# Optimization experiments

Hardware: AMD Instinct MI355X
Metric: run time of the kernel (lower is better)

The kernel has to match this reference:

```python
import jax, jax.numpy as jnp
import numpy as np

HIDDEN = 2048
EXPERTS = 8
INTER = 1024
TOP_K = 2
AUX_LOSS_WEIGHT = 0.01
TOKENS = 8192


def setup_inputs() -> dict:
    key = jax.random.key(0)
    k_x, k_g, k_w1, k_w2 = jax.random.split(key, 4)
    x = jax.random.normal(k_x, (TOKENS, HIDDEN), dtype=jnp.float32)
    # nn.Linear(hidden, experts, bias=False): weight is [E, H], applied as x @ W^T
    gate_w = jax.random.normal(k_g, (EXPERTS, HIDDEN), dtype=jnp.float32) * 0.02
    w1 = jax.random.normal(k_w1, (EXPERTS, HIDDEN, INTER), dtype=jnp.float32) * 0.02
    w2 = jax.random.normal(k_w2, (EXPERTS, INTER, HIDDEN), dtype=jnp.float32) * 0.02
    return {"x": x, "gate_w": gate_w, "w1": w1, "w2": w2}


def _moe_forward(x, gate_w, w1, w2):
    E = gate_w.shape[0]
    logits = x @ gate_w.T                              # [T, E]
    probs = jax.nn.softmax(logits, axis=-1)            # [T, E]
    topk_w, topk_idx = jax.lax.top_k(probs, TOP_K)     # [T, K]
    topk_w = topk_w / jnp.sum(topk_w, axis=-1, keepdims=True)

    # load-balancing aux loss: E * sum_e f_e * P_e
    one_hot = jax.nn.one_hot(topk_idx, E, dtype=probs.dtype)   # [T, K, E]
    f = jnp.mean(jnp.sum(one_hot, axis=1), axis=0)             # fraction of tokens per expert
    P = jnp.mean(probs, axis=0)                                # mean router prob per expert
    aux_loss = AUX_LOSS_WEIGHT * E * jnp.sum(f * P)

    # grouped expert MLP (dense-over-experts formulation, same math as
    # permute -> grouped GEMM -> unpermute):
    h = jnp.einsum('th,ehi->tei', x, w1)               # [T, E, I]
    h = jax.nn.gelu(h)
    y = jnp.einsum('tei,eih->teh', h, w2)              # [T, E, H]

    # combine: gather each token's top-k expert outputs and weight them
    y_sel = jnp.take_along_axis(y, topk_idx[:, :, None], axis=1)  # [T, K, H]
    out = jnp.sum(y_sel * topk_w[:, :, None], axis=1)             # [T, H]
    return out, aux_loss


def reference(x, gate_w, w1, w2):
    return _moe_forward(x, gate_w, w1, w2)
```

## Files before the change

kernel.cpp:

```cpp
#include <hip/hip_runtime.h>
#include <hip/hip_fp16.h>
#include <cmath>

#define T_TOKENS 8192
#define HID 2048
#define NEXP 8
#define INTERM 1024
#define GATE_NB 2048

typedef _Float16 f16x8 __attribute__((ext_vector_type(8)));
typedef _Float16 f16x4 __attribute__((ext_vector_type(4)));
typedef float f32x4 __attribute__((ext_vector_type(4)));

static __device__ __forceinline__ float gelu_tanh(float v) {
    return 0.5f * v * (1.0f + tanhf(0.79788456080286535588f * (v + 0.044715f * v * v * v)));
}

static __device__ __forceinline__ void glds16(const void* g, void* l) {
    __builtin_amdgcn_global_load_lds((const __attribute__((address_space(1))) void*)g,
                                     (__attribute__((address_space(3))) void*)l, 16, 0, 0);
}

__global__ __launch_bounds__(256) void tconv_kernel(const float* __restrict__ in,
                                                    _Float16* __restrict__ out,
                                                    int R, int C) {
    __shared__ float t[32][33];
    int z = blockIdx.z;
    int r0 = blockIdx.y * 32, c0 = blockIdx.x * 32;
    int tid = threadIdx.x;
    int r = tid >> 3, c4 = (tid & 7) * 4;
    const float4 v = *reinterpret_cast<const float4*>(&in[((size_t)z * R + (r0 + r)) * C + c0 + c4]);
    t[r][c4 + 0] = v.x; t[r][c4 + 1] = v.y; t[r][c4 + 2] = v.z; t[r][c4 + 3] = v.w;
    __syncthreads();
    int oc = tid >> 3;
    int or4 = (tid & 7) * 4;
    f16x4 o;
    o[0] = (_Float16)t[or4 + 0][oc];
    o[1] = (_Float16)t[or4 + 1][oc];
    o[2] = (_Float16)t[or4 + 2][oc];
    o[3] = (_Float16)t[or4 + 3][oc];
    *reinterpret_cast<f16x4*>(&out[((size_t)z * C + (c0 + oc)) * R + r0 + or4]) = o;
}

__global__ __launch_bounds__(256) void gate_kernel(const float* __restrict__ x,
                                                   const float* __restrict__ gw,
                                                   _Float16* __restrict__ xh,
                                                   int* __restrict__ tk_idx, float* __restrict__ tk_w,
                                                   int* __restrict__ part_cnt,
                                                   double* __restrict__ part_sumP)
{
    __shared__ double sds[4][NEXP];
    __shared__ int sci[4][NEXP];
    int w = threadIdx.x >> 6;
    int lane = threadIdx.x & 63;
    int t = blockIdx.x * 4 + w;

    const float4* xr = (const float4*)(x + (size_t)t * HID);
    _Float16* xo = xh + (size_t)t * HID;
    double acc[NEXP];
#pragma unroll
    for (int e = 0; e < NEXP; e++) acc[e] = 0.0;
#pragma unroll
    for (int i = 0; i < HID / 256; i++) {
        float4 xv = xr[i * 64 + lane];
        f16x4 h;
        h[0] = (_Float16)xv.x; h[1] = (_Float16)xv.y;
        h[2] = (_Float16)xv.z; h[3] = (_Float16)xv.w;
        *reinterpret_cast<f16x4*>(xo + i * 256 + lane * 4) = h;
#pragma unroll
        for (int e = 0; e < NEXP; e++) {
            float4 gv = ((const float4*)(gw + (size_t)e * HID))[i * 64 + lane];
            acc[e] += (double)xv.x * (double)gv.x + (double)xv.y * (double)gv.y
                    + (double)xv.z * (double)gv.z + (double)xv.w * (double)gv.w;
        }
    }
#pragma unroll
    for (int e = 0; e < NEXP; e++) {
#pragma unroll
        for (int off = 32; off > 0; off >>= 1) acc[e] += __shfl_xor(acc[e], off, 64);
    }
    double mx = acc[0];
#pragma unroll
    for (int e = 1; e < NEXP; e++) mx = acc[e] > mx ? acc[e] : mx;
    double ex[NEXP];
    double sum = 0.0;
#pragma unroll
    for (int e = 0; e < NEXP; e++) { ex[e] = exp(acc[e] - mx); sum += ex[e]; }
    int i0 = 0;
#pragma unroll
    for (int e = 1; e < NEXP; e++) if (ex[e] > ex[i0]) i0 = e;
    int i1 = (i0 == 0) ? 1 : 0;
#pragma unroll
    for (int e = 0; e < NEXP; e++) if (e != i0 && ex[e] > ex[i1]) i1 = e;
    double p0 = ex[i0], p1 = ex[i1];
    double t2 = p0 + p1;
    if (lane == 0) {
        tk_idx[2 * t] = i0; tk_idx[2 * t + 1] = i1;
        tk_w[2 * t] = (float)(p0 / t2); tk_w[2 * t + 1] = (float)(p1 / t2);
#pragma unroll
        for (int e = 0; e < NEXP; e++) {
            sds[w][e] = ex[e] / sum;
            sci[w][e] = (e == i0 ? 1 : 0) + (e == i1 ? 1 : 0);
        }
    }
    __syncthreads();
    if (threadIdx.x < NEXP) {
        int e = threadIdx.x;
        part_sumP[e * GATE_NB + blockIdx.x] = sds[0][e] + sds[1][e] + sds[2][e] + sds[3][e];
        part_cnt[e * GATE_NB + blockIdx.x]  = sci[0][e] + sci[1][e] + sci[2][e] + sci[3][e];
    }
}

__global__ __launch_bounds__(256) void finalize_kernel(const int* __restrict__ part_cnt,
                                                       const double* __restrict__ part_sumP,
                                                       int* __restrict__ cnt, int* __restrict__ offs,
                                                       int* __restrict__ cursor,
                                                       float* __restrict__ aux_out) {
    __shared__ double swv[4];
    __shared__ int cwv[4];
    __shared__ double sE[NEXP];
    __shared__ int cE[NEXP];
    int w = threadIdx.x >> 6;
    int lane = threadIdx.x & 63;
    for (int e = 0; e < NEXP; e++) {
        double s = 0.0; int c = 0;
        for (int j = threadIdx.x; j < GATE_NB; j += 256) {
            s += part_sumP[e * GATE_NB + j];
            c += part_cnt[e * GATE_NB + j];
        }
#pragma unroll
        for (int off = 32; off > 0; off >>= 1) {
            s += __shfl_xor(s, off, 64);
            c += __shfl_xor(c, off, 64);
        }
        if (lane == 0) { swv[w] = s; cwv[w] = c; }
        __syncthreads();
        if (threadIdx.x == 0) {
            sE[e] = swv[0] + swv[1] + swv[2] + swv[3];
            cE[e] = cwv[0] + cwv[1] + cwv[2] + cwv[3];
        }
        __syncthreads();
    }
    if (threadIdx.x == 0) {
        int off = 0;
        double aux = 0.0;
#pragma unroll
        for (int e = 0; e < NEXP; e++) {
            cnt[e] = cE[e];
            offs[e] = off;
            off += cE[e];
            cursor[e] = 0;
            aux += ((double)cE[e] / (double)T_TOKENS) * (sE[e] / (double)T_TOKENS);
        }
        aux_out[0] = (float)(0.01 * (double)NEXP * aux);
    }
}

__global__ void scatter_kernel(const int* __restrict__ tk_idx, const float* __restrict__ tk_w,
                               const int* __restrict__ offs, int* __restrict__ cursor,
                               int* __restrict__ row_tok, float* __restrict__ row_w,
                               int* __restrict__ tok_row) {
    int t = blockIdx.x * blockDim.x + threadIdx.x;
    int lane = threadIdx.x & 63;
    unsigned long long below = (lane == 0) ? 0ull : ((~0ull) >> (64 - lane));
    for (int k = 0; k < 2; k++) {
        int e = tk_idx[2 * t + k];
        float wv = tk_w[2 * t + k];
        int pos = 0;
#pragma unroll
        for (int ee = 0; ee < NEXP; ee++) {
            unsigned long long m = __ballot(e == ee);
            if (e == ee) {
                int rank = (int)__popcll(m & below);
                int leader = (int)__ffsll((unsigned long long)m) - 1;
                int base = 0;
                if (lane == leader) base = atomicAdd(&cursor[ee], (int)__popcll(m));
                base = __shfl(base, leader, 64);
                pos = base + rank;
            }
        }
        int r = offs[e] + pos;
        row_tok[r] = t;
        row_w[r] = wv;
        tok_row[2 * t + k] = r;
    }
}

__global__ __launch_bounds__(256) void gemm1_kernel(const _Float16* __restrict__ xh,
                                                    const _Float16* __restrict__ w1t,
                                                    const int* __restrict__ cnt, const int* __restrict__ offs,
                                                    const int* __restrict__ row_tok,
                                                    _Float16* __restrict__ hh) {
    int e = blockIdx.z;
    int Ne = cnt[e];
    int m0 = blockIdx.y * 128;
    if (m0 >= Ne) return;
    int base = offs[e];
    int n0 = blockIdx.x * 128;

    __shared__ __align__(16) _Float16 As[128][32];
    __shared__ __align__(16) _Float16 Bs[128][32];

    int tid = threadIdx.x;
    int lane = tid & 63;
    int w = tid >> 6, wm = w >> 1, wn = w & 1;

    int r0 = lane >> 2;
    int kh = (((lane & 3) ^ ((lane >> 3) & 3))) * 8;
    int rowA0 = m0 + w * 32 + r0;      if (rowA0 >= Ne) rowA0 = Ne - 1;
    int rowA1 = m0 + w * 32 + 16 + r0; if (rowA1 >= Ne) rowA1 = Ne - 1;
    int tok0 = row_tok[base + rowA0];
    int tok1 = row_tok[base + rowA1];
    const _Float16* aSrc0 = xh + (size_t)tok0 * HID + kh;
    const _Float16* aSrc1 = xh + (size_t)tok1 * HID + kh;
    const _Float16* bSrc0 = w1t + ((size_t)e * INTERM + n0 + w * 32 + r0) * HID + kh;
    const _Float16* bSrc1 = w1t + ((size_t)e * INTERM + n0 + w * 32 + 16 + r0) * HID + kh;
    _Float16* ldsA0 = &As[w * 32][0];
    _Float16* ldsA1 = &As[w * 32 + 16][0];
    _Float16* ldsB0 = &Bs[w * 32][0];
    _Float16* ldsB1 = &Bs[w * 32 + 16][0];

    f32x4 acc[4][4] = {};
    int fr = lane & 15;
    int fq = lane >> 4;
    int fk = (fq ^ ((fr >> 1) & 3)) * 8;

    for (int k0 = 0; k0 < HID; k0 += 32) {
        glds16(aSrc0 + k0, ldsA0);
        glds16(aSrc1 + k0, ldsA1);
        glds16(bSrc0 + k0, ldsB0);
        glds16(bSrc1 + k0, ldsB1);
        __syncthreads();
        f16x8 a[4], b[4];
#pragma unroll
        for (int mi = 0; mi < 4; mi++) a[mi] = *(const f16x8*)&As[wm * 64 + mi * 16 + fr][fk];
#pragma unroll
        for (int ni = 0; ni < 4; ni++) b[ni] = *(const f16x8*)&Bs[wn * 64 + ni * 16 + fr][fk];
#pragma unroll
        for (int mi = 0; mi < 4; mi++)
#pragma unroll
            for (int ni = 0; ni < 4; ni++)
                acc[mi][ni] = __builtin_amdgcn_mfma_f32_16x16x32_f16(a[mi], b[ni], acc[mi][ni], 0, 0, 0);
        __syncthreads();
    }

    int fq4 = fq * 4;
#pragma unroll
    for (int mi = 0; mi < 4; mi++) {
#pragma unroll
        for (int r = 0; r < 4; r++) {
            int row = m0 + wm * 64 + mi * 16 + fq4 + r;
            if (row < Ne) {
                _Float16* dst = hh + (size_t)(base + row) * INTERM + n0 + wn * 64 + fr;
#pragma unroll
                for (int ni = 0; ni < 4; ni++)
                    dst[ni * 16] = (_Float16)gelu_tanh(acc[mi][ni][r]);
            }
        }
    }
}

__global__ __launch_bounds__(256) void gemm2_kernel(const _Float16* __restrict__ hh,
                                                    const _Float16* __restrict__ w2t,
                                                    const int* __restrict__ cnt, const int* __restrict__ offs,
                                                    _Float16* __restrict__ y) {
    int e = blockIdx.z;
    int Ne = cnt[e];
    int m0 = blockIdx.y * 128;
    if (m0 >= Ne) return;
    int base = offs[e];
    int n0 = blockIdx.x * 128;

    __shared__ __align__(16) _Float16 As[128][32];
    __shared__ __align__(16) _Float16 Bs[128][32];

    int tid = threadIdx.x;
    int lane = tid & 63;
    int w = tid >> 6, wm = w >> 1, wn = w & 1;

    int r0 = lane >> 2;
    int kh = (((lane & 3) ^ ((lane >> 3) & 3))) * 8;
    int rowA0 = m0 + w * 32 + r0;      if (rowA0 >= Ne) rowA0 = Ne - 1;
    int rowA1 = m0 + w * 32 + 16 + r0; if (rowA1 >= Ne) rowA1 = Ne - 1;
    const _Float16* aSrc0 = hh + (size_t)(base + rowA0) * INTERM + kh;
    const _Float16* aSrc1 = hh + (size_t)(base + rowA1) * INTERM + kh;
    const _Float16* bSrc0 = w2t + ((size_t)e * HID + n0 + w * 32 + r0) * INTERM + kh;
    const _Float16* bSrc1 = w2t + ((size_t)e * HID + n0 + w * 32 + 16 + r0) * INTERM + kh;
    _Float16* ldsA0 = &As[w * 32][0];
    _Float16* ldsA1 = &As[w * 32 + 16][0];
    _Float16* ldsB0 = &Bs[w * 32][0];
    _Float16* ldsB1 = &Bs[w * 32 + 16][0];

    f32x4 acc[4][4] = {};
    int fr = lane & 15;
    int fq = lane >> 4;
    int fk = (fq ^ ((fr >> 1) & 3)) * 8;

    for (int k0 = 0; k0 < INTERM; k0 += 32) {
        glds16(aSrc0 + k0, ldsA0);
        glds16(aSrc1 + k0, ldsA1);
        glds16(bSrc0 + k0, ldsB0);
        glds16(bSrc1 + k0, ldsB1);
        __syncthreads();
        f16x8 a[4], b[4];
#pragma unroll
        for (int mi = 0; mi < 4; mi++) a[mi] = *(const f16x8*)&As[wm * 64 + mi * 16 + fr][fk];
#pragma unroll
        for (int ni = 0; ni < 4; ni++) b[ni] = *(const f16x8*)&Bs[wn * 64 + ni * 16 + fr][fk];
#pragma unroll
        for (int mi = 0; mi < 4; mi++)
#pragma unroll
            for (int ni = 0; ni < 4; ni++)
                acc[mi][ni] = __builtin_amdgcn_mfma_f32_16x16x32_f16(a[mi], b[ni], acc[mi][ni], 0, 0, 0);
        __syncthreads();
    }

    int fq4 = fq * 4;
#pragma unroll
    for (int mi = 0; mi < 4; mi++) {
#pragma unroll
        for (int r = 0; r < 4; r++) {
            int row = m0 + wm * 64 + mi * 16 + fq4 + r;
            if (row < Ne) {
                _Float16* dst = y + (size_t)(base + row) * HID + n0 + wn * 64 + fr;
#pragma unroll
                for (int ni = 0; ni < 4; ni++)
                    dst[ni * 16] = (_Float16)acc[mi][ni][r];
            }
        }
    }
}

__global__ __launch_bounds__(256) void combine_kernel(const _Float16* __restrict__ y,
                                                      const int* __restrict__ tok_row,
                                                      const float* __restrict__ tk_w,
                                                      float* __restrict__ out) {
    int t = blockIdx.x;
    int c = threadIdx.x;
    int r0 = tok_row[2 * t], r1 = tok_row[2 * t + 1];
    float w0 = tk_w[2 * t], w1 = tk_w[2 * t + 1];
    f16x8 a = reinterpret_cast<const f16x8*>(y + (size_t)r0 * HID)[c];
    f16x8 b = reinterpret_cast<const f16x8*>(y + (size_t)r1 * HID)[c];
    float4 o0, o1;
    o0.x = w0 * (float)a[0] + w1 * (float)b[0];
    o0.y = w0 * (float)a[1] + w1 * (float)b[1];
    o0.z = w0 * (float)a[2] + w1 * (float)b[2];
    o0.w = w0 * (float)a[3] + w1 * (float)b[3];
    o1.x = w0 * (float)a[4] + w1 * (float)b[4];
    o1.y = w0 * (float)a[5] + w1 * (float)b[5];
    o1.z = w0 * (float)a[6] + w1 * (float)b[6];
    o1.w = w0 * (float)a[7] + w1 * (float)b[7];
    float4* dst = reinterpret_cast<float4*>(out + (size_t)t * HID + c * 8);
    dst[0] = o0;
    dst[1] = o1;
}

extern "C" void kernel_launch(void* const* d_in, const int* in_sizes, int n_in,
                              void* d_out, int out_size, void* d_ws, size_t ws_size,
                              hipStream_t stream) {
    const float* x  = (const float*)d_in[0];
    const float* gw = (const float*)d_in[1];
    const float* w1 = (const float*)d_in[2];
    const float* w2 = (const float*)d_in[3];
    float* out = (float*)d_out;
    char* ws = (char*)d_ws;

    int*    cnt       = (int*)(ws + 0);
    int*    cursor    = (int*)(ws + 64);
    int*    offs      = (int*)(ws + 128);
    int*    part_cnt  = (int*)(ws + 4096);
    double* part_sumP = (double*)(ws + 131072);
    int*    row_tok   = (int*)(ws + 262144);
    float*  row_w     = (float*)(ws + 327680);
    int*    tk_idx    = (int*)(ws + 393216);
    float*  tk_w      = (float*)(ws + 458752);
    int*    tok_row   = (int*)(ws + 524288);
    const size_t OFF = 589824;
    _Float16* xh  = (_Float16*)(ws + OFF);
    _Float16* w1t = (_Float16*)(ws + OFF + (1ull << 25));
    _Float16* w2t = (_Float16*)(ws + OFF + (2ull << 25));
    _Float16* hh  = (_Float16*)(ws + OFF + (3ull << 25));
    _Float16* y   = (_Float16*)(ws + OFF);

    dim3 g1(INTERM / 32, HID / 32, NEXP);
    tconv_kernel<<<g1, 256, 0, stream>>>(w1, w1t, HID, INTERM);
    dim3 g2(HID / 32, INTERM / 32, NEXP);
    tconv_kernel<<<g2, 256, 0, stream>>>(w2, w2t, INTERM, HID);

    gate_kernel<<<GATE_NB, 256, 0, stream>>>(x, gw, xh, tk_idx, tk_w, part_cnt, part_sumP);
    finalize_kernel<<<1, 256, 0, stream>>>(part_cnt, part_sumP, cnt, offs, cursor,
                                           out + (size_t)T_TOKENS * HID);
    scatter_kernel<<<T_TOKENS / 256, 256, 0, stream>>>(tk_idx, tk_w, offs, cursor,
                                                       row_tok, row_w, tok_row);

    dim3 gg1(INTERM / 128, 64, NEXP);
    gemm1_kernel<<<gg1, 256, 0, stream>>>(xh, w1t, cnt, offs, row_tok, hh);
    dim3 gg2(HID / 128, 64, NEXP);
    gemm2_kernel<<<gg2, 256, 0, stream>>>(hh, w2t, cnt, offs, y);

    combine_kernel<<<T_TOKENS, 256, 0, stream>>>(y, tok_row, tk_w, out);
}
```

Baseline: 409.4 us.

## Replace expert GEMMs with 256x256 double-buffered, 8-wave pipelined MFMA kernel

Merges the two grouped expert GEMMs into one templated kernel that uses 256x256 output tiles, 8 waves, a K-step of 64 and double-buffered LDS fed by global_load_lds prefetch. The prefetch is interleaved with four compute phases, and each phase uses explicit barriers, waitcnt and setprio so that loads overlap the MFMA work. The LDS layout gets an XOR swizzle over 16-byte chunks to avoid bank conflicts. This aims to raise MFMA utilisation and data reuse, at the cost of 128KB of LDS per block, higher register pressure and more wasted work on padded tiles when experts receive few tokens.

```diff
diff --git a/kernel.cpp b/kernel.cpp
--- a/kernel.cpp
+++ b/kernel.cpp
@@ -19,6 +19,12 @@
 static __device__ __forceinline__ void glds16(const void* g, void* l) {
     __builtin_amdgcn_global_load_lds((const __attribute__((address_space(1))) void*)g,
                                      (__attribute__((address_space(3))) void*)l, 16, 0, 0);
+}
+
+static __device__ __forceinline__ f16x8 lds_read(const _Float16* base, int row, int chunk) {
+    int phys = chunk ^ (row & 7);
+    return *reinterpret_cast<const f16x8*>(
+        reinterpret_cast<const char*>(base) + row * 128 + phys * 16);
 }
 
 __global__ __launch_bounds__(256) void tconv_kernel(const float* __restrict__ in,
@@ -47,8 +53,7 @@
                                                    _Float16* __restrict__ xh,
                                                    int* __restrict__ tk_idx, float* __restrict__ tk_w,
                                                    int* __restrict__ part_cnt,
-                                                   double* __restrict__ part_sumP)
-{
+                                                   double* __restrict__ part_sumP) {
     __shared__ double sds[4][NEXP];
     __shared__ int sci[4][NEXP];
     int w = threadIdx.x >> 6;
@@ -173,10 +178,10 @@
             if (e == ee) {
                 int rank = (int)__popcll(m & below);
                 int leader = (int)__ffsll((unsigned long long)m) - 1;
-                int base = 0;
-                if (lane == leader) base = atomicAdd(&cursor[ee], (int)__popcll(m));
-                base = __shfl(base, leader, 64);
-                pos = base + rank;
+                int b = 0;
+                if (lane == leader) b = atomicAdd(&cursor[ee], (int)__popcll(m));
+                b = __shfl(b, leader, 64);
+                pos = b + rank;
             }
         }
         int r = offs[e] + pos;
@@ -186,146 +191,125 @@
     }
 }
 
-__global__ __launch_bounds__(256) void gemm1_kernel(const _Float16* __restrict__ xh,
-                                                    const _Float16* __restrict__ w1t,
-                                                    const int* __restrict__ cnt, const int* __restrict__ offs,
-                                                    const int* __restrict__ row_tok,
-                                                    _Float16* __restrict__ hh) {
+#define DO_PHASE(MH, NH, EXTRA) do {                                                   \
+    f16x8 a_[4][2], b_[2][2];                                                          \
+    _Pragma("unroll") for (int i_ = 0; i_ < 4; i_++)                                   \
+    _Pragma("unroll") for (int k_ = 0; k_ < 2; k_++)                                   \
+        a_[i_][k_] = lds_read(Ab, wr * 128 + ((MH) * 4 + i_) * 16 + fr, k_ * 4 + fq);  \
+    _Pragma("unroll") for (int j_ = 0; j_ < 2; j_++)                                   \
+    _Pragma("unroll") for (int k_ = 0; k_ < 2; k_++)                                   \
+        b_[j_][k_] = lds_read(Bb, wc * 64 + ((NH) * 2 + j_) * 16 + fr, k_ * 4 + fq);   \
+    EXTRA                                                                              \
+    __builtin_amdgcn_s_barrier();                                                      \
+    asm volatile("s_waitcnt lgkmcnt(0)" ::: "memory");                                 \
+    __builtin_amdgcn_s_setprio(1);                                                     \
+    _Pragma("unroll") for (int i_ = 0; i_ < 4; i_++)                                   \
+    _Pragma("unroll") for (int j_ = 0; j_ < 2; j_++)                                   \
+    _Pragma("unroll") for (int k_ = 0; k_ < 2; k_++)                                   \
+        acc[(MH) * 4 + i_][(NH) * 2 + j_] = __builtin_amdgcn_mfma_f32_16x16x32_f16(    \
+            a_[i_][k_], b_[j_][k_], acc[(MH) * 4 + i_][(NH) * 2 + j_], 0, 0, 0);       \
+    __builtin_amdgcn_s_setprio(0);                                                     \
+    __builtin_amdgcn_s_barrier();                                                      \
+} while (0)
+
+template<bool GATHER, bool GELU, int KTOT>
+__global__ __launch_bounds__(512, 2) void gemm8_kernel(
+    const _Float16* __restrict__ Aglob,
+    const _Float16* __restrict__ Bglob,
+    const int* __restrict__ cnt, const int* __restrict__ offs,
+    const int* __restrict__ row_tok,
+    _Float16* __restrict__ Out, int Ncols)
+{
+    constexpr int NT = KTOT / 64;
     int e = blockIdx.z;
     int Ne = cnt[e];
-    int m0 = blockIdx.y * 128;
+    int m0 = blockIdx.y * 256;
     if (m0 >= Ne) return;
     int base = offs[e];
-    int n0 = blockIdx.x * 128;
-
-    __shared__ __align__(16) _Float16 As[128][32];
-    __shared__ __align__(16) _Float16 Bs[128][32];
+    int n0 = blockIdx.x * 256;
+
+    __shared__ __align__(16) _Float16 As[2][256][64];
+    __shared__ __align__(16) _Float16 Bs[2][256][64];
 
     int tid = threadIdx.x;
+    int w = tid >> 6;
     int lane = tid & 63;
-    int w = tid >> 6, wm = w >> 1, wn = w & 1;
-
-    int r0 = lane >> 2;
-    int kh = (((lane & 3) ^ ((lane >> 3) & 3))) * 8;
-    int rowA0 = m0 + w * 32 + r0;      if (rowA0 >= Ne) rowA0 = Ne - 1;
-    int rowA1 = m0 + w * 32 + 16 + r0; if (rowA1 >= Ne) rowA1 = Ne - 1;
-    int tok0 = row_tok[base + rowA0];
-    int tok1 = row_tok[base + rowA1];
-    const _Float16* aSrc0 = xh + (size_t)tok0 * HID + kh;
-    const _Float16* aSrc1 = xh + (size_t)tok1 * HID + kh;
-    const _Float16* bSrc0 = w1t + ((size_t)e * INTERM + n0 + w * 32 + r0) * HID + kh;
-    const _Float16* bSrc1 = w1t + ((size_t)e * INTERM + n0 + w * 32 + 16 + r0) * HID + kh;
-    _Float16* ldsA0 = &As[w * 32][0];
-    _Float16* ldsA1 = &As[w * 32 + 16][0];
-    _Float16* ldsB0 = &Bs[w * 32][0];
-    _Float16* ldsB1 = &Bs[w * 32 + 16][0];
-
-    f32x4 acc[4][4] = {};
-    int fr = lane & 15;
-    int fq = lane >> 4;
-    int fk = (fq ^ ((fr >> 1) & 3)) * 8;
-
-    for (int k0 = 0; k0 < HID; k0 += 32) {
-        glds16(aSrc0 + k0, ldsA0);
-        glds16(aSrc1 + k0, ldsA1);
-        glds16(bSrc0 + k0, ldsB0);
-        glds16(bSrc1 + k0, ldsB1);
-        __syncthreads();
-        f16x8 a[4], b[4];
-#pragma unroll
-        for (int mi = 0; mi < 4; mi++) a[mi] = *(const f16x8*)&As[wm * 64 + mi * 16 + fr][fk];
-#pragma unroll
-        for (int ni = 0; ni < 4; ni++) b[ni] = *(const f16x8*)&Bs[wn * 64 + ni * 16 + fr][fk];
-#pragma unroll
-        for (int mi = 0; mi < 4; mi++)
-#pragma unroll
-            for (int ni = 0; ni < 4; ni++)
-                acc[mi][ni] = __builtin_amdgcn_mfma_f32_16x16x32_f16(a[mi], b[ni], acc[mi][ni], 0, 0, 0);
-        __syncthreads();
-    }
-
-    int fq4 = fq * 4;
-#pragma unroll
-    for (int mi = 0; mi < 4; mi++) {
+    int wr = w >> 2, wc = w & 3;
+    int fr = lane & 15, fq = lane >> 4;
+
+    int trow = tid >> 3;
+    int lc = (tid & 7) ^ (trow & 7);
+    int ar0 = m0 + 0 * 64 + trow; if (ar0 >= Ne) ar0 = Ne - 1;
+    int ar1 = m0 + 1 * 64 + trow; if (ar1 >= Ne) ar1 = Ne - 1;
+    int ar2 = m0 + 2 * 64 + trow; if (ar2 >= Ne) ar2 = Ne - 1;
+    int ar3 = m0 + 3 * 64 + trow; if (ar3 >= Ne) ar3 = Ne - 1;
+    int id0 = GATHER ? row_tok[base + ar0] : (base + ar0);
+    int id1 = GATHER ? row_tok[base + ar1] : (base + ar1);
+    int id2 = GATHER ? row_tok[base + ar2] : (base + ar2);
+    int id3 = GATHER ? row_tok[base + ar3] : (base + ar3);
+    const _Float16* aSrc0 = Aglob + (size_t)id0 * KTOT + lc * 8;
+    const _Float16* aSrc1 = Aglob + (size_t)id1 * KTOT + lc * 8;
+    const _Float16* aSrc2 = Aglob + (size_t)id2 * KTOT + lc * 8;
+    const _Float16* aSrc3 = Aglob + (size_t)id3 * KTOT + lc * 8;
+    const size_t bexp = (size_t)e * Ncols * KTOT;
+    const _Float16* bSrc0 = Bglob + bexp + (size_t)(n0 + 0 * 64 + trow) * KTOT + lc * 8;
+    const _Float16* bSrc1 = Bglob + bexp + (size_t)(n0 + 1 * 64 + trow) * KTOT + lc * 8;
+    const _Float16* bSrc2 = Bglob + bexp + (size_t)(n0 + 2 * 64 + trow) * KTOT + lc * 8;
+    const _Float16* bSrc3 = Bglob + bexp + (size_t)(n0 + 3 * 64 + trow) * KTOT + lc * 8;
+
+    _Float16* AsB = &As[0][0][0];
+    _Float16* BsB = &Bs[0][0][0];
+    _Float16* ldsA = AsB + w * 512;
+    _Float16* ldsB = BsB + w * 512;
+
+    f32x4 acc[8][4] = {};
+
+    glds16(aSrc0, ldsA + 0 * 4096);
+    glds16(aSrc1, ldsA + 1 * 4096);
+    glds16(aSrc2, ldsA + 2 * 4096);
+    glds16(aSrc3, ldsA + 3 * 4096);
+    glds16(bSrc0, ldsB + 0 * 4096);
+    glds16(bSrc1, ldsB + 1 * 4096);
+    glds16(bSrc2, ldsB + 2 * 4096);
+    glds16(bSrc3, ldsB + 3 * 4096);
+
+    for (int j = 0; j < NT; ++j) {
+        int slot = j & 1;
+        const _Float16* Ab = AsB + slot * 16384;
+        const _Float16* Bb = BsB + slot * 16384;
+        _Float16* An = ldsA + (slot ^ 1) * 16384;
+        _Float16* Bn = ldsB + (slot ^ 1) * 16384;
+        int koff = (j + 1) * 64;
+        bool more = (j + 1 < NT);
+        if (more) {
+            glds16(aSrc0 + koff, An + 0 * 4096);
+            glds16(aSrc1 + koff, An + 1 * 4096);
+            glds16(aSrc2 + koff, An + 2 * 4096);
+            glds16(aSrc3 + koff, An + 3 * 4096);
+            asm volatile("s_waitcnt vmcnt(4)" ::: "memory");
+        } else {
+            asm volatile("s_waitcnt vmcnt(0)" ::: "memory");
+        }
+        __builtin_amdgcn_s_barrier();
+        DO_PHASE(0, 0, if (more) { glds16(bSrc0 + koff, Bn + 0 * 4096); glds16(bSrc1 + koff, Bn + 1 * 4096); });
+        DO_PHASE(0, 1, if (more) { glds16(bSrc2 + koff, Bn + 2 * 4096); glds16(bSrc3 + koff, Bn + 3 * 4096); });
+        DO_PHASE(1, 0, );
+        DO_PHASE(1, 1, );
+    }
+
+#pragma unroll
+    for (int mi = 0; mi < 8; mi++) {
 #pragma unroll
         for (int r = 0; r < 4; r++) {
-            int row = m0 + wm * 64 + mi * 16 + fq4 + r;
+            int row = m0 + wr * 128 + mi * 16 + fq * 4 + r;
             if (row < Ne) {
-                _Float16* dst = hh + (size_t)(base + row) * INTERM + n0 + wn * 64 + fr;
-#pragma unroll
-                for (int ni = 0; ni < 4; ni++)
-                    dst[ni * 16] = (_Float16)gelu_tanh(acc[mi][ni][r]);
-            }
-        }
-    }
-}
-
-__global__ __launch_bounds__(256) void gemm2_kernel(const _Float16* __restrict__ hh,
-                                                    const _Float16* __restrict__ w2t,
-                                                    const int* __restrict__ cnt, const int* __restrict__ offs,
-                                                    _Float16* __restrict__ y) {
-    int e = blockIdx.z;
-    int Ne = cnt[e];
-    int m0 = blockIdx.y * 128;
-    if (m0 >= Ne) return;
-    int base = offs[e];
-    int n0 = blockIdx.x * 128;
-
-    __shared__ __align__(16) _Float16 As[128][32];
-    __shared__ __align__(16) _Float16 Bs[128][32];
-
-    int tid = threadIdx.x;
-    int lane = tid & 63;
-    int w = tid >> 6, wm = w >> 1, wn = w & 1;
-
-    int r0 = lane >> 2;
-    int kh = (((lane & 3) ^ ((lane >> 3) & 3))) * 8;
-    int rowA0 = m0 + w * 32 + r0;      if (rowA0 >= Ne) rowA0 = Ne - 1;
-    int rowA1 = m0 + w * 32 + 16 + r0; if (rowA1 >= Ne) rowA1 = Ne - 1;
-    const _Float16* aSrc0 = hh + (size_t)(base + rowA0) * INTERM + kh;
-    const _Float16* aSrc1 = hh + (size_t)(base + rowA1) * INTERM + kh;
-    const _Float16* bSrc0 = w2t + ((size_t)e * HID + n0 + w * 32 + r0) * INTERM + kh;
-    const _Float16* bSrc1 = w2t + ((size_t)e * HID + n0 + w * 32 + 16 + r0) * INTERM + kh;
-    _Float16* ldsA0 = &As[w * 32][0];
-    _Float16* ldsA1 = &As[w * 32 + 16][0];
-    _Float16* ldsB0 = &Bs[w * 32][0];
-    _Float16* ldsB1 = &Bs[w * 32 + 16][0];
-
-    f32x4 acc[4][4] = {};
-    int fr = lane & 15;
-    int fq = lane >> 4;
-    int fk = (fq ^ ((fr >> 1) & 3)) * 8;
-
-    for (int k0 = 0; k0 < INTERM; k0 += 32) {
-        glds16(aSrc0 + k0, ldsA0);
-        glds16(aSrc1 + k0, ldsA1);
-        glds16(bSrc0 + k0, ldsB0);
-        glds16(bSrc1 + k0, ldsB1);
-        __syncthreads();
-        f16x8 a[4], b[4];
-#pragma unroll
-        for (int mi = 0; mi < 4; mi++) a[mi] = *(const f16x8*)&As[wm * 64 + mi * 16 + fr][fk];
-#pragma unroll
-        for (int ni = 0; ni < 4; ni++) b[ni] = *(const f16x8*)&Bs[wn * 64 + ni * 16 + fr][fk];
-#pragma unroll
-        for (int mi = 0; mi < 4; mi++)
-#pragma unroll
-            for (int ni = 0; ni < 4; ni++)
-                acc[mi][ni] = __builtin_amdgcn_mfma_f32_16x16x32_f16(a[mi], b[ni], acc[mi][ni], 0, 0, 0);
-        __syncthreads();
-    }
-
-    int fq4 = fq * 4;
-#pragma unroll
-    for (int mi = 0; mi < 4; mi++) {
-#pragma unroll
-        for (int r = 0; r < 4; r++) {
-            int row = m0 + wm * 64 + mi * 16 + fq4 + r;
-            if (row < Ne) {
-                _Float16* dst = y + (size_t)(base + row) * HID + n0 + wn * 64 + fr;
-#pragma unroll
-                for (int ni = 0; ni < 4; ni++)
-                    dst[ni * 16] = (_Float16)acc[mi][ni][r];
+                _Float16* dst = Out + (size_t)(base + row) * Ncols + n0 + wc * 64 + fr;
+#pragma unroll
+                for (int ni = 0; ni < 4; ni++) {
+                    float v = acc[mi][ni][r];
+                    if (GELU) v = gelu_tanh(v);
+                    dst[ni * 16] = (_Float16)v;
+                }
             }
         }
     }
@@ -393,10 +377,10 @@
     scatter_kernel<<<T_TOKENS / 256, 256, 0, stream>>>(tk_idx, tk_w, offs, cursor,
                                                        row_tok, row_w, tok_row);
 
-    dim3 gg1(INTERM / 128, 64, NEXP);
-    gemm1_kernel<<<gg1, 256, 0, stream>>>(xh, w1t, cnt, offs, row_tok, hh);
-    dim3 gg2(HID / 128, 64, NEXP);
-    gemm2_kernel<<<gg2, 256, 0, stream>>>(hh, w2t, cnt, offs, y);
+    dim3 gg1(INTERM / 256, 32, NEXP);
+    gemm8_kernel<true, true, HID><<<gg1, 512, 0, stream>>>(xh, w1t, cnt, offs, row_tok, hh, INTERM);
+    dim3 gg2(HID / 256, 32, NEXP);
+    gemm8_kernel<false, false, INTERM><<<gg2, 512, 0, stream>>>(hh, w2t, cnt, offs, row_tok, y, HID);
 
     combine_kernel<<<T_TOKENS, 256, 0, stream>>>(y, tok_row, tk_w, out);
 }
```

New measurement: 474.6 us. +15.9%, slower.
